# Optimization experiments

Measured on AMD Instinct MI355X. Metric: run time of the kernel, lower is better.

## Reference

```python
import jax, jax.numpy as jnp
import numpy as np


def _mlp(x, W1, b1, W2, b2):
    # Dropout layers are identity at inference (p=0.2 in train only).
    h = jax.nn.relu(jnp.einsum('bsi,ih->bsh', x, W1) + b1)
    return jax.nn.relu(jnp.einsum('bsh,hk->bsk', h, W2) + b2)


def setup_inputs() -> dict:
    key = jax.random.key(0)
    ks = jax.random.split(key, 4)
    B_, S, D_in, H = 32, 1024, 768, 1024
    A = jax.random.normal(ks[0], (B_, S, D_in), dtype=jnp.float32)
    B = jax.random.normal(ks[1], (B_, S, D_in), dtype=jnp.float32)
    W1 = jax.random.normal(ks[2], (D_in, H), dtype=jnp.float32) * (1.0 / np.sqrt(D_in))
    b1 = jnp.zeros((H,), dtype=jnp.float32)
    W2 = jax.random.normal(ks[3], (H, H), dtype=jnp.float32) * (1.0 / np.sqrt(H))
    b2 = jnp.zeros((H,), dtype=jnp.float32)
    return {"A": A, "B": B, "W1": W1, "b1": b1, "W2": W2, "b2": b2}


def reference(A, B, W1, b1, W2, b2):
    f_A = _mlp(A, W1, b1, W2, b2)           # [b, S, H]
    f_B = _mlp(B, W1, b1, W2, b2)           # [b, S, H]
    e = jnp.einsum('bih,bjh->bij', f_A, f_B)  # [b, S_A, S_B] unscaled scores
    beta = jnp.einsum('bij,bjd->bid', jax.nn.softmax(e, axis=-1), B)
    # alpha = softmax(e^T, -1) @ B  (note: B, exactly as in the source code)
    alpha = jnp.einsum('bji,bjd->bid', jax.nn.softmax(jnp.swapaxes(e, 1, 2), axis=-1), B)
    return (beta, alpha)
```

## Files before the change

### kernel.cpp

```cpp
#include <hip/hip_runtime.h>
#include <hip/hip_bf16.h>

typedef __attribute__((ext_vector_type(8))) short bf16x8;
typedef __attribute__((ext_vector_type(4))) float f32x4;

__device__ __forceinline__ unsigned short f2bf(float f) {
  union { float f; unsigned u; } v; v.f = f;
  unsigned r = v.u + 0x7FFFu + ((v.u >> 16) & 1u);
  return (unsigned short)(r >> 16);
}

__device__ __forceinline__ void gl_lds16(const void* g, void* l) {
  __builtin_amdgcn_global_load_lds(
      (__attribute__((address_space(1))) void*)(g),
      (__attribute__((address_space(3))) void*)(l), 16, 0, 0);
}

__global__ __launch_bounds__(256) void k_convert(const float* __restrict__ in,
                                                 unsigned short* __restrict__ out,
                                                 int n8) {
  int i = blockIdx.x * 256 + threadIdx.x;
  if (i >= n8) return;
  const float4* ip = (const float4*)in;
  float4 v0 = ip[2 * i], v1 = ip[2 * i + 1];
  ushort4 o0 = make_ushort4(f2bf(v0.x), f2bf(v0.y), f2bf(v0.z), f2bf(v0.w));
  ushort4 o1 = make_ushort4(f2bf(v1.x), f2bf(v1.y), f2bf(v1.z), f2bf(v1.w));
  ((ushort4*)out)[2 * i] = o0;
  ((ushort4*)out)[2 * i + 1] = o1;
}

template <typename OutT>
__global__ __launch_bounds__(256) void k_transpose(const float* __restrict__ in,
                                                   OutT* __restrict__ out,
                                                   int R, int C,
                                                   long inStride, long outStride) {
  __shared__ float tile[64][65];
  const float* ib = in + (long)blockIdx.z * inStride;
  OutT* ob = out + (long)blockIdx.z * outStride;
  int tc = blockIdx.x * 64;
  int tr = blockIdx.y * 64;
  int t = threadIdx.x;
  int lr = t >> 4;
  int lc = (t & 15) * 4;
#pragma unroll
  for (int rr = 0; rr < 64; rr += 16) {
    float4 v = *(const float4*)&ib[(long)(tr + rr + lr) * C + tc + lc];
    tile[rr + lr][lc + 0] = v.x;
    tile[rr + lr][lc + 1] = v.y;
    tile[rr + lr][lc + 2] = v.z;
    tile[rr + lr][lc + 3] = v.w;
  }
  __syncthreads();
#pragma unroll
  for (int ii = 0; ii < 64; ii += 16) {
    int i = ii + lr;
    if constexpr (sizeof(OutT) == 2) {
      ushort4 w = make_ushort4(f2bf(tile[lc + 0][i]), f2bf(tile[lc + 1][i]),
                               f2bf(tile[lc + 2][i]), f2bf(tile[lc + 3][i]));
      *(ushort4*)&ob[(long)(tc + i) * R + tr + lc] = w;
    } else {
      float4 w = make_float4(tile[lc + 0][i], tile[lc + 1][i],
                             tile[lc + 2][i], tile[lc + 3][i]);
      *(float4*)&ob[(long)(tc + i) * R + tr + lc] = w;
    }
  }
}

__global__ __launch_bounds__(256) void k_colstats(const float* __restrict__ E,
                                                  float* __restrict__ colMp,
                                                  float* __restrict__ colSp) {
  const float* e = E + (long)blockIdx.y * 1048576L + (long)blockIdx.x * 131072L +
                   threadIdx.x * 4;
  float m0 = -3.4e38f, m1 = -3.4e38f, m2 = -3.4e38f, m3 = -3.4e38f;
  float s0 = 0.f, s1 = 0.f, s2 = 0.f, s3 = 0.f;
  for (int r = 0; r < 128; ++r) {
    float4 v = *(const float4*)(e + (long)r * 1024);
    float n0 = fmaxf(m0, v.x); s0 = s0 * __expf(m0 - n0) + __expf(v.x - n0); m0 = n0;
    float n1 = fmaxf(m1, v.y); s1 = s1 * __expf(m1 - n1) + __expf(v.y - n1); m1 = n1;
    float n2 = fmaxf(m2, v.z); s2 = s2 * __expf(m2 - n2) + __expf(v.z - n2); m2 = n2;
    float n3 = fmaxf(m3, v.w); s3 = s3 * __expf(m3 - n3) + __expf(v.w - n3); m3 = n3;
  }
  long o = ((long)blockIdx.y * 8 + blockIdx.x) * 1024 + threadIdx.x * 4;
  *(float4*)&colMp[o] = make_float4(m0, m1, m2, m3);
  *(float4*)&colSp[o] = make_float4(s0, s1, s2, s3);
}

__global__ __launch_bounds__(256) void k_colcombine(const float* __restrict__ colMp,
                                                    const float* __restrict__ colSp,
                                                    float* __restrict__ colM,
                                                    float* __restrict__ colIS) {
  int idx = blockIdx.x * 256 + threadIdx.x;
  int b = idx >> 10, c = idx & 1023;
  float m = -3.4e38f;
  float mc[8], sc[8];
#pragma unroll
  for (int k = 0; k < 8; ++k) {
    mc[k] = colMp[((long)b * 8 + k) * 1024 + c];
    sc[k] = colSp[((long)b * 8 + k) * 1024 + c];
    m = fmaxf(m, mc[k]);
  }
  float s = 0.f;
#pragma unroll
  for (int k = 0; k < 8; ++k) s += sc[k] * __expf(mc[k] - m);
  colM[idx] = m;
  colIS[idx] = 1.0f / s;
}

__global__ __launch_bounds__(256) void k_softmax(const float* __restrict__ E,
                                                 unsigned short* __restrict__ P,
                                                 unsigned short* __restrict__ P2,
                                                 const float* __restrict__ colM,
                                                 const float* __restrict__ colIS) {
  long row = blockIdx.x;
  const float* e = E + row * 1024;
  int t = threadIdx.x;
  float4 v = *(const float4*)&e[t * 4];
  float m = fmaxf(fmaxf(v.x, v.y), fmaxf(v.z, v.w));
#pragma unroll
  for (int o = 32; o; o >>= 1) m = fmaxf(m, __shfl_xor(m, o));
  __shared__ float red[4];
  __shared__ float red2[4];
  int wid = t >> 6;
  if ((t & 63) == 0) red[wid] = m;
  __syncthreads();
  m = fmaxf(fmaxf(red[0], red[1]), fmaxf(red[2], red[3]));
  float p0 = __expf(v.x - m), p1 = __expf(v.y - m);
  float p2 = __expf(v.z - m), p3 = __expf(v.w - m);
  float s = p0 + p1 + p2 + p3;
#pragma unroll
  for (int o = 32; o; o >>= 1) s += __shfl_xor(s, o);
  if ((t & 63) == 0) red2[wid] = s;
  __syncthreads();
  s = red2[0] + red2[1] + red2[2] + red2[3];
  float inv = 1.0f / s;
  *(ushort4*)&P[row * 1024 + t * 4] =
      make_ushort4(f2bf(p0 * inv), f2bf(p1 * inv), f2bf(p2 * inv), f2bf(p3 * inv));
  long cb = (row >> 10) * 1024 + t * 4;
  float4 cm = *(const float4*)&colM[cb];
  float4 ci = *(const float4*)&colIS[cb];
  *(ushort4*)&P2[row * 1024 + t * 4] =
      make_ushort4(f2bf(__expf(v.x - cm.x) * ci.x), f2bf(__expf(v.y - cm.y) * ci.y),
                   f2bf(__expf(v.z - cm.z) * ci.z), f2bf(__expf(v.w - cm.w) * ci.w));
}

template <bool BIAS_RELU, bool OUT_BF16>
__global__ __launch_bounds__(256, 4) void k_gemm_bt(
    const unsigned short* __restrict__ A, long lda, long aBatch,
    const unsigned short* __restrict__ Bt, long ldb, long bBatch,
    void* __restrict__ C, long ldc, long cBatch,
    const float* __restrict__ bias, int K) {
  __shared__ unsigned short As[128 * 32];
  __shared__ unsigned short Bs[128 * 32];
  const int t = threadIdx.x;
  const int w = t >> 6, l = t & 63;
  const int lr = l & 15, lh = l >> 4;
  const int wr = w >> 1, wc = w & 1;

  const int gx = gridDim.x, gy = gridDim.y;
  const int nwg = gx * gy * gridDim.z;
  const int hw = blockIdx.x + gx * (blockIdx.y + gy * blockIdx.z);
  const int q = nwg >> 3;
  const int logical = (hw & 7) * q + (hw >> 3);
  const int bx = logical % gx;
  const int rem = logical / gx;
  const int by = rem % gy;
  const int bz = rem / gy;

  const long m0 = (long)by * 128;
  const long n0 = (long)bx * 128;
  const unsigned short* Ab = A + (long)bz * aBatch;
  const unsigned short* Bb = Bt + (long)bz * bBatch;

  const int ca0 = w * 2, ca1 = w * 2 + 1;
  const int srow = l >> 2;
  const int sc16 = (l & 3) ^ ((srow >> 1) & 3);
  const int scol = sc16 * 8;
  const unsigned short* ag0 = Ab + (m0 + ca0 * 16 + srow) * lda + scol;
  const unsigned short* ag1 = Ab + (m0 + ca1 * 16 + srow) * lda + scol;
  const unsigned short* bg0 = Bb + (n0 + ca0 * 16 + srow) * ldb + scol;
  const unsigned short* bg1 = Bb + (n0 + ca1 * 16 + srow) * ldb + scol;
  unsigned short* al0 = &As[ca0 * 512];
  unsigned short* al1 = &As[ca1 * 512];
  unsigned short* bl0 = &Bs[ca0 * 512];
  unsigned short* bl1 = &Bs[ca1 * 512];

  f32x4 acc[4][4];
#pragma unroll
  for (int i = 0; i < 4; ++i)
#pragma unroll
    for (int j = 0; j < 4; ++j) acc[i][j] = (f32x4){0.f, 0.f, 0.f, 0.f};

  const int rswz = ((lr >> 1) & 3) * 8;

  for (int k0 = 0; k0 < K; k0 += 32) {
    gl_lds16(ag0 + k0, al0);
    gl_lds16(ag1 + k0, al1);
    gl_lds16(bg0 + k0, bl0);
    gl_lds16(bg1 + k0, bl1);
    __syncthreads();
    bf16x8 af[4], bfr[4];
#pragma unroll
    for (int m = 0; m < 4; ++m)
      af[m] = *(const bf16x8*)&As[(wr * 64 + m * 16 + lr) * 32 + ((lh * 8) ^ rswz)];
#pragma unroll
    for (int n = 0; n < 4; ++n)
      bfr[n] = *(const bf16x8*)&Bs[(wc * 64 + n * 16 + lr) * 32 + ((lh * 8) ^ rswz)];
#pragma unroll
    for (int m = 0; m < 4; ++m)
#pragma unroll
      for (int n = 0; n < 4; ++n)
        acc[m][n] = __builtin_amdgcn_mfma_f32_16x16x32_bf16(af[m], bfr[n], acc[m][n], 0, 0, 0);
    __syncthreads();
  }

  const long crow = m0 + wr * 64;
  const long ccol = n0 + wc * 64;
#pragma unroll
  for (int n = 0; n < 4; ++n) {
    const long col = ccol + n * 16 + lr;
    float bv = 0.f;
    if constexpr (BIAS_RELU) bv = bias[col];
#pragma unroll
    for (int m = 0; m < 4; ++m) {
      f32x4 v = acc[m][n];
#pragma unroll
      for (int r = 0; r < 4; ++r) {
        const long rrow = crow + m * 16 + lh * 4 + r;
        float x = v[r];
        if constexpr (BIAS_RELU) x = fmaxf(x + bv, 0.f);
        if constexpr (OUT_BF16)
          ((unsigned short*)C)[(long)bz * cBatch + rrow * ldc + col] = f2bf(x);
        else
          ((float*)C)[(long)bz * cBatch + rrow * ldc + col] = x;
      }
    }
  }
}

extern "C" void kernel_launch(void* const* d_in, const int* in_sizes, int n_in,
                              void* d_out, int out_size, void* d_ws, size_t ws_size,
                              hipStream_t stream) {
  const float* A_in = (const float*)d_in[0];
  const float* B_in = (const float*)d_in[1];
  const float* W1 = (const float*)d_in[2];
  const float* b1 = (const float*)d_in[3];
  const float* W2 = (const float*)d_in[4];
  const float* b2 = (const float*)d_in[5];

  char* ws = (char*)d_ws;
  unsigned short* Xbf  = (unsigned short*)(ws + 0L);
  unsigned short* H    = (unsigned short*)(ws + 100663296L);
  unsigned short* F    = (unsigned short*)(ws + 234881024L);
  unsigned short* BinT = (unsigned short*)(ws + 369098752L);
  unsigned short* W1T  = (unsigned short*)(ws + 419430400L);
  unsigned short* W2T  = (unsigned short*)(ws + 421003264L);
  unsigned short* P    = (unsigned short*)(ws + 0L);
  unsigned short* P2   = (unsigned short*)(ws + 234881024L);
  float* colMp = (float*)(ws + 100663296L);
  float* colSp = (float*)(ws + 100663296L + 1048576L);
  float* colM  = (float*)(ws + 100663296L + 2097152L);
  float* colIS = (float*)(ws + 100663296L + 2228224L);
  float* E  = (float*)d_out;
  float* beta = (float*)d_out;
  float* alpha = (float*)d_out + 25165824L;

  k_convert<<<12288, 256, 0, stream>>>(A_in, Xbf, 3145728);
  k_convert<<<12288, 256, 0, stream>>>(B_in, Xbf + 25165824L, 3145728);
  k_transpose<unsigned short><<<dim3(16, 12, 1), 256, 0, stream>>>(W1, W1T, 768, 1024, 0, 0);
  k_transpose<unsigned short><<<dim3(16, 16, 1), 256, 0, stream>>>(W2, W2T, 1024, 1024, 0, 0);
  k_transpose<unsigned short><<<dim3(12, 16, 32), 256, 0, stream>>>(B_in, BinT, 1024, 768, 786432L, 786432L);

  k_gemm_bt<true, true><<<dim3(8, 512, 1), 256, 0, stream>>>(
      Xbf, 768, 0, W1T, 768, 0, (void*)H, 1024, 0, b1, 768);
  k_gemm_bt<true, true><<<dim3(8, 512, 1), 256, 0, stream>>>(
      H, 1024, 0, W2T, 1024, 0, (void*)F, 1024, 0, b2, 1024);

  k_gemm_bt<false, false><<<dim3(8, 8, 32), 256, 0, stream>>>(
      F, 1024, 1048576L, F + 33554432L, 1024, 1048576L, (void*)E, 1024, 1048576L, nullptr, 1024);

  k_colstats<<<dim3(8, 32), 256, 0, stream>>>(E, colMp, colSp);
  k_colcombine<<<128, 256, 0, stream>>>(colMp, colSp, colM, colIS);
  k_softmax<<<32768, 256, 0, stream>>>(E, P, P2, colM, colIS);

  k_gemm_bt<false, false><<<dim3(6, 8, 32), 256, 0, stream>>>(
      P, 1024, 1048576L, BinT, 1024, 786432L, (void*)beta, 768, 786432L, nullptr, 1024);
  k_gemm_bt<false, false><<<dim3(6, 8, 32), 256, 0, stream>>>(
      P2, 1024, 1048576L, BinT, 1024, 786432L, (void*)alpha, 768, 786432L, nullptr, 1024);
}
```

Measured before the change: 769.2 us.

## Replace 128x128 GEMM with double-buffered 256x256 tile kernel using 8 waves

The bf16 MFMA GEMM moves from 128x128x32 tiles with 4 waves and a single LDS buffer to 256x256x64 tiles with 8 waves and double-buffered LDS. The next tile's global-to-LDS loads are issued ahead and overlapped with compute, using explicit vmcnt waits, split barriers and setprio. The larger tile raises data reuse per load and cuts the number of workgroups. The cost is 128 KB of LDS per block and more accumulator registers, which lowers occupancy, and fewer blocks for the smaller batched GEMMs (384 for the output GEMMs).

```diff
diff --git a/kernel.cpp b/kernel.cpp
--- a/kernel.cpp
+++ b/kernel.cpp
@@ -144,17 +144,17 @@
 }
 
 template <bool BIAS_RELU, bool OUT_BF16>
-__global__ __launch_bounds__(256, 4) void k_gemm_bt(
+__global__ __launch_bounds__(512, 2) void k_gemm256(
     const unsigned short* __restrict__ A, long lda, long aBatch,
     const unsigned short* __restrict__ Bt, long ldb, long bBatch,
     void* __restrict__ C, long ldc, long cBatch,
     const float* __restrict__ bias, int K) {
-  __shared__ unsigned short As[128 * 32];
-  __shared__ unsigned short Bs[128 * 32];
+  __shared__ unsigned short As[2][16384];
+  __shared__ unsigned short Bs[2][16384];
   const int t = threadIdx.x;
   const int w = t >> 6, l = t & 63;
   const int lr = l & 15, lh = l >> 4;
-  const int wr = w >> 1, wc = w & 1;
+  const int wr = w >> 2, wc = w & 3;
 
   const int gx = gridDim.x, gy = gridDim.y;
   const int nwg = gx * gy * gridDim.z;
@@ -166,72 +166,98 @@
   const int by = rem % gy;
   const int bz = rem / gy;
 
-  const long m0 = (long)by * 128;
-  const long n0 = (long)bx * 128;
-  const unsigned short* Ab = A + (long)bz * aBatch;
-  const unsigned short* Bb = Bt + (long)bz * bBatch;
-
-  const int ca0 = w * 2, ca1 = w * 2 + 1;
-  const int srow = l >> 2;
-  const int sc16 = (l & 3) ^ ((srow >> 1) & 3);
-  const int scol = sc16 * 8;
-  const unsigned short* ag0 = Ab + (m0 + ca0 * 16 + srow) * lda + scol;
-  const unsigned short* ag1 = Ab + (m0 + ca1 * 16 + srow) * lda + scol;
-  const unsigned short* bg0 = Bb + (n0 + ca0 * 16 + srow) * ldb + scol;
-  const unsigned short* bg1 = Bb + (n0 + ca1 * 16 + srow) * ldb + scol;
-  unsigned short* al0 = &As[ca0 * 512];
-  unsigned short* al1 = &As[ca1 * 512];
-  unsigned short* bl0 = &Bs[ca0 * 512];
-  unsigned short* bl1 = &Bs[ca1 * 512];
-
-  f32x4 acc[4][4];
-#pragma unroll
-  for (int i = 0; i < 4; ++i)
+  const long m0 = (long)by * 256;
+  const long n0 = (long)bx * 256;
+  const unsigned short* Ab = A + (long)bz * aBatch + m0 * lda;
+  const unsigned short* Bb = Bt + (long)bz * bBatch + n0 * ldb;
+
+  const int sgrow8 = l >> 3;
+  const int wrow = w * 8 + sgrow8;
+  const int scol = ((l & 7) ^ sgrow8) * 8;
+
+  auto stA = [&](int buf, int win, int k0) {
+    gl_lds16(Ab + (long)(win + wrow) * lda + k0 + scol,
+             &As[buf][(win + w * 8) * 64]);
+  };
+  auto stB = [&](int buf, int win, int k0) {
+    gl_lds16(Bb + (long)(win + wrow) * ldb + k0 + scol,
+             &Bs[buf][(win + w * 8) * 64]);
+  };
+
+  f32x4 acc[8][4];
+#pragma unroll
+  for (int i = 0; i < 8; ++i)
 #pragma unroll
     for (int j = 0; j < 4; ++j) acc[i][j] = (f32x4){0.f, 0.f, 0.f, 0.f};
 
-  const int rswz = ((lr >> 1) & 3) * 8;
-
-  for (int k0 = 0; k0 < K; k0 += 32) {
-    gl_lds16(ag0 + k0, al0);
-    gl_lds16(ag1 + k0, al1);
-    gl_lds16(bg0 + k0, bl0);
-    gl_lds16(bg1 + k0, bl1);
-    __syncthreads();
-    bf16x8 af[4], bfr[4];
-#pragma unroll
-    for (int m = 0; m < 4; ++m)
-      af[m] = *(const bf16x8*)&As[(wr * 64 + m * 16 + lr) * 32 + ((lh * 8) ^ rswz)];
-#pragma unroll
-    for (int n = 0; n < 4; ++n)
-      bfr[n] = *(const bf16x8*)&Bs[(wc * 64 + n * 16 + lr) * 32 + ((lh * 8) ^ rswz)];
-#pragma unroll
-    for (int m = 0; m < 4; ++m)
-#pragma unroll
-      for (int n = 0; n < 4; ++n)
-        acc[m][n] = __builtin_amdgcn_mfma_f32_16x16x32_bf16(af[m], bfr[n], acc[m][n], 0, 0, 0);
-    __syncthreads();
-  }
-
-  const long crow = m0 + wr * 64;
-  const long ccol = n0 + wc * 64;
+  int sw[2];
+#pragma unroll
+  for (int kk = 0; kk < 2; ++kk) sw[kk] = ((kk * 4 + lh) ^ (lr & 7)) * 8;
+
+#define PHASE(MQ, NQ)                                                          \
+  {                                                                            \
+    bf16x8 af[4][2], bfr[2][2];                                                \
+    _Pragma("unroll") for (int mm = 0; mm < 4; ++mm)                           \
+      _Pragma("unroll") for (int kk = 0; kk < 2; ++kk)                         \
+        af[mm][kk] = *(const bf16x8*)&Ac[(wr * 128 + ((MQ)*4 + mm) * 16 + lr) * 64 + sw[kk]]; \
+    _Pragma("unroll") for (int nn = 0; nn < 2; ++nn)                           \
+      _Pragma("unroll") for (int kk = 0; kk < 2; ++kk)                         \
+        bfr[nn][kk] = *(const bf16x8*)&Bc[(wc * 64 + ((NQ)*2 + nn) * 16 + lr) * 64 + sw[kk]]; \
+    asm volatile("s_barrier" ::: "memory");                                    \
+    __builtin_amdgcn_s_setprio(1);                                             \
+    _Pragma("unroll") for (int mm = 0; mm < 4; ++mm)                           \
+      _Pragma("unroll") for (int nn = 0; nn < 2; ++nn)                         \
+        _Pragma("unroll") for (int kk = 0; kk < 2; ++kk)                       \
+          acc[(MQ)*4 + mm][(NQ)*2 + nn] = __builtin_amdgcn_mfma_f32_16x16x32_bf16( \
+              af[mm][kk], bfr[nn][kk], acc[(MQ)*4 + mm][(NQ)*2 + nn], 0, 0, 0); \
+    __builtin_amdgcn_s_setprio(0);                                             \
+    asm volatile("s_barrier" ::: "memory");                                    \
+  }
+
+  const int NT = K >> 6;
+  stA(0, 0, 0); stA(0, 64, 0); stA(0, 128, 0); stA(0, 192, 0);
+  stB(0, 0, 0); stB(0, 64, 0); stB(0, 128, 0); stB(0, 192, 0);
+
+  for (int tt = 0; tt < NT; ++tt) {
+    const int cur = tt & 1;
+    const int nxt = cur ^ 1;
+    const unsigned short* Ac = As[cur];
+    const unsigned short* Bc = Bs[cur];
+    const int kn = (tt + 1) << 6;
+    if (tt + 1 < NT) {
+      stA(nxt, 0, kn); stA(nxt, 64, kn); stA(nxt, 128, kn); stA(nxt, 192, kn);
+      stB(nxt, 0, kn); stB(nxt, 64, kn);
+      asm volatile("s_waitcnt vmcnt(6)" ::: "memory");
+    } else {
+      asm volatile("s_waitcnt vmcnt(0)" ::: "memory");
+    }
+    asm volatile("s_barrier" ::: "memory");
+    PHASE(0, 0);
+    if (tt + 1 < NT) { stB(nxt, 128, kn); stB(nxt, 192, kn); }
+    PHASE(0, 1);
+    PHASE(1, 0);
+    PHASE(1, 1);
+  }
+#undef PHASE
+
+  const long crow0 = m0 + wr * 128;
+  const long ccol0 = n0 + wc * 64;
 #pragma unroll
   for (int n = 0; n < 4; ++n) {
-    const long col = ccol + n * 16 + lr;
+    const long col = ccol0 + n * 16 + lr;
     float bv = 0.f;
     if constexpr (BIAS_RELU) bv = bias[col];
 #pragma unroll
-    for (int m = 0; m < 4; ++m) {
-      f32x4 v = acc[m][n];
+    for (int m = 0; m < 8; ++m) {
 #pragma unroll
       for (int r = 0; r < 4; ++r) {
-        const long rrow = crow + m * 16 + lh * 4 + r;
-        float x = v[r];
+        const long row = crow0 + m * 16 + lh * 4 + r;
+        float x = acc[m][n][r];
         if constexpr (BIAS_RELU) x = fmaxf(x + bv, 0.f);
         if constexpr (OUT_BF16)
-          ((unsigned short*)C)[(long)bz * cBatch + rrow * ldc + col] = f2bf(x);
+          ((unsigned short*)C)[(long)bz * cBatch + row * ldc + col] = f2bf(x);
         else
-          ((float*)C)[(long)bz * cBatch + rrow * ldc + col] = x;
+          ((float*)C)[(long)bz * cBatch + row * ldc + col] = x;
       }
     }
   }
@@ -270,20 +296,20 @@
   k_transpose<unsigned short><<<dim3(16, 16, 1), 256, 0, stream>>>(W2, W2T, 1024, 1024, 0, 0);
   k_transpose<unsigned short><<<dim3(12, 16, 32), 256, 0, stream>>>(B_in, BinT, 1024, 768, 786432L, 786432L);
 
-  k_gemm_bt<true, true><<<dim3(8, 512, 1), 256, 0, stream>>>(
+  k_gemm256<true, true><<<dim3(4, 256, 1), 512, 0, stream>>>(
       Xbf, 768, 0, W1T, 768, 0, (void*)H, 1024, 0, b1, 768);
-  k_gemm_bt<true, true><<<dim3(8, 512, 1), 256, 0, stream>>>(
+  k_gemm256<true, true><<<dim3(4, 256, 1), 512, 0, stream>>>(
       H, 1024, 0, W2T, 1024, 0, (void*)F, 1024, 0, b2, 1024);
 
-  k_gemm_bt<false, false><<<dim3(8, 8, 32), 256, 0, stream>>>(
+  k_gemm256<false, false><<<dim3(4, 4, 32), 512, 0, stream>>>(
       F, 1024, 1048576L, F + 33554432L, 1024, 1048576L, (void*)E, 1024, 1048576L, nullptr, 1024);
 
   k_colstats<<<dim3(8, 32), 256, 0, stream>>>(E, colMp, colSp);
   k_colcombine<<<128, 256, 0, stream>>>(colMp, colSp, colM, colIS);
   k_softmax<<<32768, 256, 0, stream>>>(E, P, P2, colM, colIS);
 
-  k_gemm_bt<false, false><<<dim3(6, 8, 32), 256, 0, stream>>>(
+  k_gemm256<false, false><<<dim3(3, 4, 32), 512, 0, stream>>>(
       P, 1024, 1048576L, BinT, 1024, 786432L, (void*)beta, 768, 786432L, nullptr, 1024);
-  k_gemm_bt<false, false><<<dim3(6, 8, 32), 256, 0, stream>>>(
+  k_gemm256<false, false><<<dim3(3, 4, 32), 512, 0, stream>>>(
       P2, 1024, 1048576L, BinT, 1024, 786432L, (void*)alpha, 768, 786432L, nullptr, 1024);
 }
```

Measured after the change: 973.1 us. 1.26x slower.
